# Optimization experiments

Hardware: AMD Instinct MI355X
Metric: run time of the kernel (lower is better)

Reference implementation:

```python
import jax, jax.numpy as jnp
import numpy as np

B, T, P = 8192, 1024, 12  # series, timesteps, seasonal_period
INIT_ALPHA = 0.5 / P


def setup_inputs() -> dict:
    key = jax.random.key(0)
    k1, k2, k3, k4 = jax.random.split(key, 4)
    # positive data/states to keep multiplicative-season divisions well-conditioned
    y = jax.random.uniform(k1, (B, T, 1), dtype=jnp.float32) + 0.5
    l0 = jax.random.uniform(k2, (B, 1), dtype=jnp.float32) + 0.5
    b0 = jax.random.uniform(k3, (B, 1), dtype=jnp.float32) * 0.1
    s0 = jax.random.uniform(k4, (B, P), dtype=jnp.float32) + 0.5
    # learned smoothing params, shape (input_dim=1, 1) as in build()
    alpha = jnp.full((1, 1), INIT_ALPHA, dtype=jnp.float32)
    beta = jnp.full((1, 1), 0.1 * INIT_ALPHA, dtype=jnp.float32)
    phi = jnp.full((1, 1), 0.99, dtype=jnp.float32)
    gamma = jnp.full((1, 1), 0.05 * INIT_ALPHA, dtype=jnp.float32)
    return {"y": y, "l0": l0, "b0": b0, "s0": s0,
            "alpha": alpha, "beta": beta, "phi": phi, "gamma": gamma}


def reference(y, l0, b0, s0, alpha, beta, phi, gamma):
    # Holt-Winters ES recurrence: additive trend, multiplicative season.
    def step(carry, yt):  # yt: [B,1]
        l_prev, b_prev, s_prev = carry
        l = alpha * yt / s_prev[:, :1] + (1.0 - alpha) * (l_prev + phi * b_prev)
        b = beta * (l - l_prev) + (1.0 - beta) * b_prev * phi
        c = gamma * yt / l + (1.0 - gamma) * s_prev[:, :1]
        s = jnp.concatenate([s_prev[:, 1:], c], axis=1)  # rotate seasonal buffer
        out = (l + b * phi) * s[:, :1]
        return (l, b, s), out

    ys = jnp.swapaxes(y, 0, 1)  # [T,B,1]
    _, outs = jax.lax.scan(step, (l0, b0, s0), ys)
    return jnp.swapaxes(outs, 0, 1)  # [B,T,1]
```

## Files before the change

### kernel.cpp

```cpp
#include <hip/hip_runtime.h>


#define NS  32
#define LSY 68
#define YBW (NS * LSY)
#define LSO 36
#define OBW (64 * LSO)

typedef __attribute__((address_space(1))) const void* as1cv;
typedef __attribute__((address_space(3))) void* as3v;

template<int R>
__device__ __forceinline__ void batch16(
    const float* yb, float* ob, int base,
    float& l, float& bt, float& pn, float& rl, float* s, float* rs,
    float alpha, float oma, float beta, float nbeta, float ombphi,
    float gamma, float omg, float phi)
{
    const float4 q0 = *(const float4*)(yb + base + 0);
    const float4 q1 = *(const float4*)(yb + base + 4);
    const float4 q2 = *(const float4*)(yb + base + 8);
    const float4 q3 = *(const float4*)(yb + base + 12);
    const float yv[16] = {q0.x, q0.y, q0.z, q0.w, q1.x, q1.y, q1.z, q1.w,
                          q2.x, q2.y, q2.z, q2.w, q3.x, q3.y, q3.z, q3.w};
    float ov[16];
#pragma unroll
    for (int i = 0; i < 16; ++i) {
        const int J  = (R + i) % 12;
        const int Jn = (R + i + 1) % 12;
        const float yt = yv[i];
        const float ay = alpha * yt;
        const float a  = ay * rs[J];
        const float ln = fmaf(oma, pn, a);
        const float inner = fmaf(nbeta, l, ombphi * bt);
        const float bn  = fmaf(beta, ln, inner);
        const float pnn = fmaf(phi, bn, ln);
        rl = rl * fmaf(-ln, rl, 2.0f);
        const float gy = gamma * yt;
        const float c  = fmaf(gy, rl, omg * s[J]);
        s[J] = c;
        rs[J] = rs[J] * fmaf(-c, rs[J], 2.0f);
        ov[i] = pnn * s[Jn];
        l = ln; bt = bn; pn = pnn;
    }
#pragma unroll
    for (int i = 0; i < 16; ++i) ob[(base + i) * LSO] = ov[i];
}

#define BATCH_ARGS l, bt, pn, rl, s, rs, alpha, oma, beta, nbeta, ombphi, gamma, omg, phi

__global__ __launch_bounds__(256) void esrnn_kernel(
    const float* __restrict__ y, const float* __restrict__ l0,
    const float* __restrict__ b0, const float* __restrict__ s0,
    const float* __restrict__ alpha_p, const float* __restrict__ beta_p,
    const float* __restrict__ phi_p, const float* __restrict__ gamma_p,
    float* __restrict__ out)
{
    __shared__ float ybuf[2 * YBW];
    __shared__ float obuf[2 * OBW];

    const int tid  = threadIdx.x;
    const int wid  = tid >> 6;
    const int lane = tid & 63;

    const float alpha = alpha_p[0];
    const float beta  = beta_p[0];
    const float phi   = phi_p[0];
    const float gamma = gamma_p[0];
    const float oma    = 1.0f - alpha;
    const float omg    = 1.0f - gamma;
    const float nbeta  = -beta;
    const float ombphi = (1.0f - beta) * phi;

    const float* yg = y + (size_t)blockIdx.x * NS * 1024;

    float l = 1.0f, bt = 0.0f, pn = 1.0f, rl = 1.0f;
    float s[12], rs[12];
#pragma unroll
    for (int k = 0; k < 12; ++k) { s[k] = 1.0f; rs[k] = 1.0f; }

    if (wid == 0 && lane < NS) {
        const int b = blockIdx.x * NS + lane;
        l  = l0[b];
        bt = b0[b];
        const float4 s03 = *(const float4*)(s0 + b * 12);
        const float4 s47 = *(const float4*)(s0 + b * 12 + 4);
        const float4 s8b = *(const float4*)(s0 + b * 12 + 8);
        s[0] = s03.x; s[1] = s03.y; s[2]  = s03.z; s[3]  = s03.w;
        s[4] = s47.x; s[5] = s47.y; s[6]  = s47.z; s[7]  = s47.w;
        s[8] = s8b.x; s[9] = s8b.y; s[10] = s8b.z; s[11] = s8b.w;
#pragma unroll
        for (int k = 0; k < 12; ++k) rs[k] = __builtin_amdgcn_rcpf(s[k]);
        rl = __builtin_amdgcn_rcpf(l);
        pn = fmaf(phi, bt, l);
    }

    for (int n = 0; n < 18; ++n) {
        if (wid == 1) {
            if (n <= 15) {
                const float* g = yg + n * 64 + lane;
                float* dst = ybuf + (size_t)(n & 1) * YBW;
#pragma unroll
                for (int r = 0; r < NS; ++r) {
                    __builtin_amdgcn_global_load_lds((as1cv)(g + r * 1024),
                                                     (as3v)(dst + r * LSY),
                                                     4, 0, 0);
                }
            }
        } else if (wid == 0) {
            if (lane < NS && n >= 1 && n <= 16) {
                const int c = n - 1;
                const float* yb = ybuf + (size_t)(c & 1) * YBW + lane * LSY;
                float*       ob = obuf + (size_t)(c & 1) * OBW + lane;
                const int m = c % 3;
                if (m == 0) {
                    batch16<0>(yb, ob, 0,  BATCH_ARGS);
                    batch16<4>(yb, ob, 16, BATCH_ARGS);
                    batch16<8>(yb, ob, 32, BATCH_ARGS);
                    batch16<0>(yb, ob, 48, BATCH_ARGS);
                } else if (m == 1) {
                    batch16<4>(yb, ob, 0,  BATCH_ARGS);
                    batch16<8>(yb, ob, 16, BATCH_ARGS);
                    batch16<0>(yb, ob, 32, BATCH_ARGS);
                    batch16<4>(yb, ob, 48, BATCH_ARGS);
                } else {
                    batch16<8>(yb, ob, 0,  BATCH_ARGS);
                    batch16<0>(yb, ob, 16, BATCH_ARGS);
                    batch16<4>(yb, ob, 32, BATCH_ARGS);
                    batch16<8>(yb, ob, 48, BATCH_ARGS);
                }
            }
        } else {
            if (n >= 2) {
                const int c = n - 2;
                const int sbase = (wid - 2) * 16;
                const float* obr = obuf + (size_t)(c & 1) * OBW
                                 + lane * LSO + sbase;
                float* og = out + (size_t)(blockIdx.x * NS + sbase) * 1024
                                + c * 64 + lane;
                float4 t0 = *(const float4*)(obr + 0);
                float4 t1 = *(const float4*)(obr + 4);
                float4 t2 = *(const float4*)(obr + 8);
                float4 t3 = *(const float4*)(obr + 12);
                og[ 0 * 1024] = t0.x; og[ 1 * 1024] = t0.y;
                og[ 2 * 1024] = t0.z; og[ 3 * 1024] = t0.w;
                og[ 4 * 1024] = t1.x; og[ 5 * 1024] = t1.y;
                og[ 6 * 1024] = t1.z; og[ 7 * 1024] = t1.w;
                og[ 8 * 1024] = t2.x; og[ 9 * 1024] = t2.y;
                og[10 * 1024] = t2.z; og[11 * 1024] = t2.w;
                og[12 * 1024] = t3.x; og[13 * 1024] = t3.y;
                og[14 * 1024] = t3.z; og[15 * 1024] = t3.w;
            }
        }
        __syncthreads();
    }
}

extern "C" void kernel_launch(void* const* d_in, const int* in_sizes, int n_in,
                              void* d_out, int out_size, void* d_ws, size_t ws_size,
                              hipStream_t stream) {
    const float* y     = (const float*)d_in[0];
    const float* l0    = (const float*)d_in[1];
    const float* b0    = (const float*)d_in[2];
    const float* s0    = (const float*)d_in[3];
    const float* alpha = (const float*)d_in[4];
    const float* beta  = (const float*)d_in[5];
    const float* phi   = (const float*)d_in[6];
    const float* gamma = (const float*)d_in[7];
    float* out = (float*)d_out;

    esrnn_kernel<<<dim3(256), dim3(256), 0, stream>>>(
        y, l0, b0, s0, alpha, beta, phi, gamma, out);
}
```

Before: 126.3 us.

## Replace per-chunk block barriers with LDS flag producer-consumer pipeline

Replaces the lockstep __syncthreads loop with warp-specialized producer/consumer roles that synchronize through LDS atomic flags. Input and output staging grows from double to quadruple buffering, so the loader, the compute warp and the two writer warps can run up to several chunks apart. The goal is to stop the serial recurrence warp from stalling on the slowest loader or writer at every barrier. It adds spin-wait polling, which uses issue slots, and relies on correct acquire/release ordering at workgroup scope.

```diff
diff --git a/kernel.cpp b/kernel.cpp
--- a/kernel.cpp
+++ b/kernel.cpp
@@ -6,9 +6,22 @@
 #define YBW (NS * LSY)
 #define LSO 36
 #define OBW (64 * LSO)
+#define NCHUNK 16
 
 typedef __attribute__((address_space(1))) const void* as1cv;
 typedef __attribute__((address_space(3))) void* as3v;
+
+__device__ __forceinline__ int ld_flag(int* f) {
+    return __hip_atomic_load(f, __ATOMIC_ACQUIRE, __HIP_MEMORY_SCOPE_WORKGROUP);
+}
+__device__ __forceinline__ void wait_ge(int* f, int target) {
+    if (target <= 0) return;
+    while (ld_flag(f) < target) {}
+}
+__device__ __forceinline__ void signal(int* f, int val, int lane) {
+    if (lane == 0)
+        __hip_atomic_store(f, val, __ATOMIC_RELEASE, __HIP_MEMORY_SCOPE_WORKGROUP);
+}
 
 template<int R>
 __device__ __forceinline__ void batch16(
@@ -56,62 +69,72 @@
     const float* __restrict__ phi_p, const float* __restrict__ gamma_p,
     float* __restrict__ out)
 {
-    __shared__ float ybuf[2 * YBW];
-    __shared__ float obuf[2 * OBW];
+    __shared__ float ybuf[4 * YBW];
+    __shared__ float obuf[4 * OBW];
+    __shared__ int   flg[4];
 
     const int tid  = threadIdx.x;
     const int wid  = tid >> 6;
     const int lane = tid & 63;
 
-    const float alpha = alpha_p[0];
-    const float beta  = beta_p[0];
-    const float phi   = phi_p[0];
-    const float gamma = gamma_p[0];
-    const float oma    = 1.0f - alpha;
-    const float omg    = 1.0f - gamma;
-    const float nbeta  = -beta;
-    const float ombphi = (1.0f - beta) * phi;
+    if (tid < 4) flg[tid] = 0;
+    __syncthreads();
 
     const float* yg = y + (size_t)blockIdx.x * NS * 1024;
 
-    float l = 1.0f, bt = 0.0f, pn = 1.0f, rl = 1.0f;
-    float s[12], rs[12];
+    if (wid == 1) {
+        for (int n = 0; n < NCHUNK; ++n) {
+            wait_ge(&flg[1], n - 3);
+            const float* g = yg + n * 64 + lane;
+            float* dst = ybuf + (size_t)(n & 3) * YBW;
 #pragma unroll
-    for (int k = 0; k < 12; ++k) { s[k] = 1.0f; rs[k] = 1.0f; }
+            for (int r = 0; r < NS; ++r) {
+                __builtin_amdgcn_global_load_lds((as1cv)(g + r * 1024),
+                                                 (as3v)(dst + r * LSY),
+                                                 4, 0, 0);
+            }
+            __builtin_amdgcn_s_waitcnt(0x0f70);
+            signal(&flg[0], n + 1, lane);
+        }
+    } else if (wid == 0) {
+        const float alpha = alpha_p[0];
+        const float beta  = beta_p[0];
+        const float phi   = phi_p[0];
+        const float gamma = gamma_p[0];
+        const float oma    = 1.0f - alpha;
+        const float omg    = 1.0f - gamma;
+        const float nbeta  = -beta;
+        const float ombphi = (1.0f - beta) * phi;
 
-    if (wid == 0 && lane < NS) {
-        const int b = blockIdx.x * NS + lane;
-        l  = l0[b];
-        bt = b0[b];
-        const float4 s03 = *(const float4*)(s0 + b * 12);
-        const float4 s47 = *(const float4*)(s0 + b * 12 + 4);
-        const float4 s8b = *(const float4*)(s0 + b * 12 + 8);
-        s[0] = s03.x; s[1] = s03.y; s[2]  = s03.z; s[3]  = s03.w;
-        s[4] = s47.x; s[5] = s47.y; s[6]  = s47.z; s[7]  = s47.w;
-        s[8] = s8b.x; s[9] = s8b.y; s[10] = s8b.z; s[11] = s8b.w;
+        float l = 1.0f, bt = 0.0f, pn = 1.0f, rl = 1.0f;
+        float s[12], rs[12];
 #pragma unroll
-        for (int k = 0; k < 12; ++k) rs[k] = __builtin_amdgcn_rcpf(s[k]);
-        rl = __builtin_amdgcn_rcpf(l);
-        pn = fmaf(phi, bt, l);
-    }
+        for (int k = 0; k < 12; ++k) { s[k] = 1.0f; rs[k] = 1.0f; }
+        if (lane < NS) {
+            const int b = blockIdx.x * NS + lane;
+            l  = l0[b];
+            bt = b0[b];
+            const float4 s03 = *(const float4*)(s0 + b * 12);
+            const float4 s47 = *(const float4*)(s0 + b * 12 + 4);
+            const float4 s8b = *(const float4*)(s0 + b * 12 + 8);
+            s[0] = s03.x; s[1] = s03.y; s[2]  = s03.z; s[3]  = s03.w;
+            s[4] = s47.x; s[5] = s47.y; s[6]  = s47.z; s[7]  = s47.w;
+            s[8] = s8b.x; s[9] = s8b.y; s[10] = s8b.z; s[11] = s8b.w;
+#pragma unroll
+            for (int k = 0; k < 12; ++k) rs[k] = __builtin_amdgcn_rcpf(s[k]);
+            rl = __builtin_amdgcn_rcpf(l);
+            pn = fmaf(phi, bt, l);
+        }
 
-    for (int n = 0; n < 18; ++n) {
-        if (wid == 1) {
-            if (n <= 15) {
-                const float* g = yg + n * 64 + lane;
-                float* dst = ybuf + (size_t)(n & 1) * YBW;
-#pragma unroll
-                for (int r = 0; r < NS; ++r) {
-                    __builtin_amdgcn_global_load_lds((as1cv)(g + r * 1024),
-                                                     (as3v)(dst + r * LSY),
-                                                     4, 0, 0);
-                }
+        for (int c = 0; c < NCHUNK; ++c) {
+            wait_ge(&flg[0], c + 1);
+            if (c >= 4) {
+                const int tgt = c - 3;
+                while (ld_flag(&flg[2]) < tgt || ld_flag(&flg[3]) < tgt) {}
             }
-        } else if (wid == 0) {
-            if (lane < NS && n >= 1 && n <= 16) {
-                const int c = n - 1;
-                const float* yb = ybuf + (size_t)(c & 1) * YBW + lane * LSY;
-                float*       ob = obuf + (size_t)(c & 1) * OBW + lane;
+            if (lane < NS) {
+                const float* yb = ybuf + (size_t)(c & 3) * YBW + lane * LSY;
+                float*       ob = obuf + (size_t)(c & 3) * OBW + lane;
                 const int m = c % 3;
                 if (m == 0) {
                     batch16<0>(yb, ob, 0,  BATCH_ARGS);
@@ -130,29 +153,31 @@
                     batch16<8>(yb, ob, 48, BATCH_ARGS);
                 }
             }
-        } else {
-            if (n >= 2) {
-                const int c = n - 2;
-                const int sbase = (wid - 2) * 16;
-                const float* obr = obuf + (size_t)(c & 1) * OBW
-                                 + lane * LSO + sbase;
-                float* og = out + (size_t)(blockIdx.x * NS + sbase) * 1024
-                                + c * 64 + lane;
-                float4 t0 = *(const float4*)(obr + 0);
-                float4 t1 = *(const float4*)(obr + 4);
-                float4 t2 = *(const float4*)(obr + 8);
-                float4 t3 = *(const float4*)(obr + 12);
-                og[ 0 * 1024] = t0.x; og[ 1 * 1024] = t0.y;
-                og[ 2 * 1024] = t0.z; og[ 3 * 1024] = t0.w;
-                og[ 4 * 1024] = t1.x; og[ 5 * 1024] = t1.y;
-                og[ 6 * 1024] = t1.z; og[ 7 * 1024] = t1.w;
-                og[ 8 * 1024] = t2.x; og[ 9 * 1024] = t2.y;
-                og[10 * 1024] = t2.z; og[11 * 1024] = t2.w;
-                og[12 * 1024] = t3.x; og[13 * 1024] = t3.y;
-                og[14 * 1024] = t3.z; og[15 * 1024] = t3.w;
-            }
+            signal(&flg[1], c + 1, lane);
         }
-        __syncthreads();
+    } else {
+        int* myf = &flg[wid];
+        const int sbase = (wid - 2) * 16;
+        for (int c = 0; c < NCHUNK; ++c) {
+            wait_ge(&flg[1], c + 1);
+            const float* obr = obuf + (size_t)(c & 3) * OBW
+                             + lane * LSO + sbase;
+            float* og = out + (size_t)(blockIdx.x * NS + sbase) * 1024
+                            + c * 64 + lane;
+            float4 t0 = *(const float4*)(obr + 0);
+            float4 t1 = *(const float4*)(obr + 4);
+            float4 t2 = *(const float4*)(obr + 8);
+            float4 t3 = *(const float4*)(obr + 12);
+            og[ 0 * 1024] = t0.x; og[ 1 * 1024] = t0.y;
+            og[ 2 * 1024] = t0.z; og[ 3 * 1024] = t0.w;
+            og[ 4 * 1024] = t1.x; og[ 5 * 1024] = t1.y;
+            og[ 6 * 1024] = t1.z; og[ 7 * 1024] = t1.w;
+            og[ 8 * 1024] = t2.x; og[ 9 * 1024] = t2.y;
+            og[10 * 1024] = t2.z; og[11 * 1024] = t2.w;
+            og[12 * 1024] = t3.x; og[13 * 1024] = t3.y;
+            og[14 * 1024] = t3.z; og[15 * 1024] = t3.w;
+            signal(myf, c + 1, lane);
+        }
     }
 }
 
```

New measurement: 123.4 us. -2.3%, faster.
